# Kernel tuning notes

Hardware: AMD Instinct MI355X
Metric: run time of the kernel (lower is better)

The kernel has to match this reference:

```python
import jax, jax.numpy as jnp
import numpy as np

V, D, B, T, S, NH, DFF, NL, PAD = 4096, 512, 32, 32, 8, 8, 2048, 4, 0


def _ln(x, g, b, eps=1e-5):
    m = jnp.mean(x, -1, keepdims=True)
    v = jnp.mean((x - m) ** 2, -1, keepdims=True)
    return (x - m) * jax.lax.rsqrt(v + eps) * g + b


def _mha(q, k, v, in_w, in_b, out_w, out_b, attn_mask=None, kpm=None):
    b_, lq, d = q.shape
    lk = k.shape[1]
    dh = d // NH
    wq, wk, wv = jnp.split(in_w, 3, 0)
    bq, bk, bv = jnp.split(in_b, 3)
    qh = (q @ wq.T + bq).reshape(b_, lq, NH, dh).transpose(0, 2, 1, 3)
    kh = (k @ wk.T + bk).reshape(b_, lk, NH, dh).transpose(0, 2, 1, 3)
    vh = (v @ wv.T + bv).reshape(b_, lk, NH, dh).transpose(0, 2, 1, 3)
    s = jnp.einsum('bhqd,bhkd->bhqk', qh, kh) * (1.0 / np.sqrt(dh))
    if attn_mask is not None:
        s = jnp.where(attn_mask[None, None], -1e9, s)
    if kpm is not None:
        s = jnp.where(kpm[:, None, None, :], -1e9, s)
    a = jax.nn.softmax(s, -1)
    o = jnp.einsum('bhqk,bhkd->bhqd', a, vh).transpose(0, 2, 1, 3).reshape(b_, lq, d)
    return o @ out_w.T + out_b


def setup_inputs():
    key = jax.random.key(0)
    ks = iter(jax.random.split(key, 48))
    nrm = lambda shape, s=0.02: jax.random.normal(next(ks), shape, jnp.float32) * s
    d = {}
    d['input_ids'] = jax.random.randint(next(ks), (B, T), 1, V)
    d['ego_info'] = jax.random.normal(next(ks), (B, 3), jnp.float32)
    d['agent_tokens'] = jax.random.randint(next(ks), (B, T, S), 1, V)
    d['agent_feats'] = jax.random.normal(next(ks), (B, T, S, 5), jnp.float32)
    d['goal'] = jax.random.randint(next(ks), (B,), 1, V)
    d['emb'] = nrm((V, D), 1.0).at[PAD].set(0.0)  # padding_idx row zeroed
    d['se_w1'] = nrm((D, D + 3)); d['se_b1'] = jnp.zeros(D)
    d['se_w2'] = nrm((D, D)); d['se_b2'] = jnp.zeros(D)
    d['be_w1'] = nrm((D, D + 5)); d['be_b1'] = jnp.zeros(D)
    d['be_w2'] = nrm((D, D)); d['be_b2'] = jnp.zeros(D)
    for nm in ('in', 'mem', 'outn'):
        d[nm + '_g'] = jnp.ones(D); d[nm + '_b'] = jnp.zeros(D)
    d['sa_in_w'] = nrm((NL, 3 * D, D)); d['sa_in_b'] = jnp.zeros((NL, 3 * D))
    d['sa_out_w'] = nrm((NL, D, D)); d['sa_out_b'] = jnp.zeros((NL, D))
    d['ca_in_w'] = nrm((NL, 3 * D, D)); d['ca_in_b'] = jnp.zeros((NL, 3 * D))
    d['ca_out_w'] = nrm((NL, D, D)); d['ca_out_b'] = jnp.zeros((NL, D))
    d['ff_w1'] = nrm((NL, DFF, D)); d['ff_b1'] = jnp.zeros((NL, DFF))
    d['ff_w2'] = nrm((NL, D, DFF)); d['ff_b2'] = jnp.zeros((NL, D))
    for nm in ('ln1', 'ln2', 'ln3'):
        d[nm + '_g'] = jnp.ones((NL, D)); d[nm + '_b'] = jnp.zeros((NL, D))
    d['proj_w'] = nrm((V, D)); d['proj_b'] = jnp.zeros(V)
    return d


def _forward(input_ids, agent_tokens, goal, ego_info, agent_feats, emb, se_w1, se_b1, se_w2, se_b2, be_w1, be_b1, be_w2, be_b2, in_g, in_b, mem_g, mem_b, outn_g, outn_b, sa_in_w, sa_in_b, sa_out_w, sa_out_b, ca_in_w, ca_in_b, ca_out_w, ca_out_b, ff_w1, ff_b1, ff_w2, ff_b2, ln1_g, ln1_b, ln2_g, ln2_b, ln3_g, ln3_b, proj_w, proj_b):
    # --- encode_self_state: embed + fuse ego features -> (B, T, D) ---
    tok = emb[input_ids]
    ego = jnp.broadcast_to(ego_info[:, None, :], (B, T, 3))
    fused = jax.nn.relu(jnp.concatenate([tok, ego], -1) @ se_w1.T + se_b1) @ se_w2.T + se_b2
    self_state = _ln(fused, in_g, in_b)
    # --- encode_agent_topology -> env (B, T, S+1, D) ---
    amask = agent_tokens != -1
    aemb = emb[jnp.where(amask, agent_tokens, PAD)]
    astate = jax.nn.relu(jnp.concatenate([aemb, agent_feats], -1) @ be_w1.T + be_b1) @ be_w2.T + be_b2
    astate = astate * amask[..., None]
    goal_e = jnp.broadcast_to(emb[goal][:, None, None, :], (B, T, 1, D))
    env = _ln(jnp.concatenate([astate, goal_e], 2), mem_g, mem_b)
    # --- windowed memory for each step t in [1, T): frames [t-2, t-1, t] clipped ---
    steps = jnp.arange(1, T)
    idx = jnp.clip(steps[:, None] + jnp.array([-2, -1, 0]), 0, T - 1)  # (T-1, 3)
    mems = env[:, idx].reshape(B, T - 1, 3 * (S + 1), D).transpose(1, 0, 2, 3)  # (T-1, B, 3A, D)
    causal = jnp.triu(jnp.ones((T, T), bool), 1)
    kpm = input_ids == PAD

    # One full-length causal decoder run per step (vmapped); identical math to the
    # original prefix loop since position t only sees keys <= t, and we read position t.
    def decode(mem):
        x = self_state
        for l in range(NL):
            x = _ln(x + _mha(x, x, x, sa_in_w[l], sa_in_b[l], sa_out_w[l], sa_out_b[l], causal, kpm), ln1_g[l], ln1_b[l])
            x = _ln(x + _mha(x, mem, mem, ca_in_w[l], ca_in_b[l], ca_out_w[l], ca_out_b[l]), ln2_g[l], ln2_b[l])
            ff = jax.nn.relu(x @ ff_w1[l].T + ff_b1[l]) @ ff_w2[l].T + ff_b2[l]
            x = _ln(x + ff, ln3_g[l], ln3_b[l])
        return x

    dec_all = jax.vmap(decode)(mems)  # (T-1, B, T, D)
    sel = dec_all[jnp.arange(T - 1), :, steps, :]  # (T-1, B, D): last position of each prefix
    logits = _ln(sel, outn_g, outn_b) @ proj_w.T + proj_b
    return jnp.transpose(logits, (1, 0, 2))  # (B, T-1, V)


def reference(input_ids, ego_info, agent_tokens, agent_feats, goal, emb, se_w1, se_b1, se_w2, se_b2, be_w1, be_b1, be_w2, be_b2, in_g, in_b, mem_g, mem_b, outn_g, outn_b, sa_in_w, sa_in_b, sa_out_w, sa_out_b, ca_in_w, ca_in_b, ca_out_w, ca_out_b, ff_w1, ff_b1, ff_w2, ff_b2, ln1_g, ln1_b, ln2_g, ln2_b, ln3_g, ln3_b, proj_w, proj_b):
    return _forward(input_ids, agent_tokens, goal, ego_info, agent_feats, emb, se_w1, se_b1, se_w2, se_b2, be_w1, be_b1, be_w2, be_b2, in_g, in_b, mem_g, mem_b, outn_g, outn_b, sa_in_w, sa_in_b, sa_out_w, sa_out_b, ca_in_w, ca_in_b, ca_out_w, ca_out_b, ff_w1, ff_b1, ff_w2, ff_b2, ln1_g, ln1_b, ln2_g, ln2_b, ln3_g, ln3_b, proj_w, proj_b)
```

## Files before the change

kernel.cpp:

```cpp
#include <hip/hip_runtime.h>
#include <hip/hip_bf16.h>
#include <stdint.h>

typedef __hip_bfloat16 bf16;
typedef __attribute__((ext_vector_type(8))) short bf16x8;
typedef __attribute__((ext_vector_type(4))) float f32x4;

__device__ __forceinline__ float b2f(bf16 v) { return __bfloat162float(v); }
__device__ __forceinline__ bf16 f2b(float v) { return __float2bfloat16(v); }
__device__ __forceinline__ unsigned short f2bu(float v) {
    bf16 h = __float2bfloat16(v);
    return *(unsigned short*)&h;
}
__device__ __forceinline__ short f2bs(float v) {
    bf16 h = __float2bfloat16(v);
    return *(short*)&h;
}
__device__ __forceinline__ float su2f(unsigned short u) {
    unsigned int x = ((unsigned int)u) << 16;
    return *(float*)&x;
}

__device__ __forceinline__ void gload_lds16(const void* g, void* l) {
    __builtin_amdgcn_global_load_lds((const __attribute__((address_space(1))) void*)g,
                                     (__attribute__((address_space(3))) void*)l, 16, 0, 0);
}

__device__ __forceinline__ int swz_byte(int row, int kk) {
    return row * 80 + 2 * (kk & 7) + 16 * ((kk >> 3) ^ (row & 3));
}

__global__ __launch_bounds__(256) void mfma_gemm(
    const bf16* __restrict__ A, const bf16* __restrict__ W,
    const float* __restrict__ bias, void* __restrict__ C,
    int M, int N, int K, int c_bf16, int relu, int store_mode)
{
    __shared__ bf16 As[128 * 64];
    __shared__ bf16 Bs[128 * 64];
    const int gx = gridDim.x;
    const int nwg = gx * gridDim.y;
    const int orig = blockIdx.y * gx + blockIdx.x;
    const int qq = nwg >> 3, rr8 = nwg & 7;
    const int xcd = orig & 7, lid = orig >> 3;
    const int wgid = (xcd < rr8 ? xcd * (qq + 1) : rr8 * (qq + 1) + (xcd - rr8) * qq) + lid;
    const int m0 = (wgid / gx) * 128, n0 = (wgid % gx) * 128;

    const int tid = threadIdx.x;
    const int wave = tid >> 6, lane = tid & 63;
    const int wr = wave >> 1, wc = wave & 1;
    const int fr = lane & 15, fg = lane >> 4;
    f32x4 acc[4][4] = {};

    const int srow = lane >> 3;
    const int sunit = (lane & 7) ^ srow;

    for (int k0 = 0; k0 < K; k0 += 64) {
#pragma unroll
        for (int c = 0; c < 4; ++c) {
            const int chunk = wave * 4 + c;
            const int arow = m0 + chunk * 8 + srow;
            const int brow = n0 + chunk * 8 + srow;
            gload_lds16(A + (size_t)arow * K + k0 + sunit * 8, (char*)As + chunk * 1024);
            gload_lds16(W + (size_t)brow * K + k0 + sunit * 8, (char*)Bs + chunk * 1024);
        }
        __syncthreads();
#pragma unroll
        for (int kk = 0; kk < 64; kk += 32) {
            bf16x8 af[4], bw[4];
            const int bo = (kk + fg * 8) * 2;
#pragma unroll
            for (int t = 0; t < 4; ++t) {
                const int ra = wr * 64 + t * 16 + fr;
                af[t] = *(const bf16x8*)((const char*)As + ra * 128 + (bo ^ ((ra & 7) << 4)));
                const int rb = wc * 64 + t * 16 + fr;
                bw[t] = *(const bf16x8*)((const char*)Bs + rb * 128 + (bo ^ ((rb & 7) << 4)));
            }
#pragma unroll
            for (int mt = 0; mt < 4; ++mt)
#pragma unroll
                for (int nt = 0; nt < 4; ++nt)
                    acc[mt][nt] = __builtin_amdgcn_mfma_f32_16x16x32_bf16(
                        af[mt], bw[nt], acc[mt][nt], 0, 0, 0);
        }
        __syncthreads();
    }
#pragma unroll
    for (int mt = 0; mt < 4; ++mt) {
#pragma unroll
        for (int r = 0; r < 4; ++r) {
            const int m = m0 + wr * 64 + mt * 16 + fg * 4 + r;
            if (m >= M) continue;
            size_t orow = (size_t)m;
            if (store_mode == 1) orow = (size_t)(m & 31) * 31 + (m >> 5);
#pragma unroll
            for (int nt = 0; nt < 4; ++nt) {
                const int n = n0 + wc * 64 + nt * 16 + fr;
                float v = acc[mt][nt][r] + bias[n];
                if (relu) v = fmaxf(v, 0.f);
                if (c_bf16) ((bf16*)C)[orow * N + n] = f2b(v);
                else        ((float*)C)[orow * N + n] = v;
            }
        }
    }
}

__global__ __launch_bounds__(256) void self_attn_mfma(
    const bf16* __restrict__ qkv, const int* __restrict__ input_ids,
    bf16* __restrict__ attn_out)
{
    const int bid = blockIdx.x;
    const int hp = bid & 3;
    const int mb = bid >> 2;
    const int b = mb & 31;
    const size_t rowbase = (size_t)mb * 32;

    __shared__ __align__(16) char vt_raw[2][64 * 80];
    __shared__ __align__(16) char ps_raw[4][16 * 80];
    __shared__ float kpmv[32];

    const int tid = threadIdx.x;
    {
        const int r = tid & 31, u = tid >> 5;
#pragma unroll
        for (int e2 = 0; e2 < 2; ++e2) {
            const int h = hp * 2 + e2;
            bf16x8 v8 = *(const bf16x8*)(qkv + (rowbase + r) * 1536 + 1024 + h * 64 + u * 8);
#pragma unroll
            for (int j = 0; j < 8; ++j)
                *(short*)(vt_raw[e2] + swz_byte(u * 8 + j, r)) = v8[j];
        }
    }
    if (tid < 32) kpmv[tid] = (input_ids[b * 32 + tid] == 0) ? -1e9f : 0.f;
    __syncthreads();

    const int wave = tid >> 6, lane = tid & 63;
    const int e = wave >> 1;
    const int h = hp * 2 + e;
    const int qi = wave & 1;
    const int c = lane & 15, fg = lane >> 4;

    const bf16* qrow = qkv + (rowbase + qi * 16 + c) * 1536 + h * 64;
    bf16x8 af0 = *(const bf16x8*)(qrow + fg * 8);
    bf16x8 af1 = *(const bf16x8*)(qrow + 32 + fg * 8);
    f32x4 s[2];
#pragma unroll
    for (int kj = 0; kj < 2; ++kj) {
        const bf16* krow = qkv + (rowbase + kj * 16 + c) * 1536 + 512 + h * 64;
        bf16x8 b0 = *(const bf16x8*)(krow + fg * 8);
        bf16x8 b1 = *(const bf16x8*)(krow + 32 + fg * 8);
        f32x4 a = {};
        a = __builtin_amdgcn_mfma_f32_16x16x32_bf16(af0, b0, a, 0, 0, 0);
        a = __builtin_amdgcn_mfma_f32_16x16x32_bf16(af1, b1, a, 0, 0, 0);
        s[kj] = a;
    }

#pragma unroll
    for (int r = 0; r < 4; ++r) {
        const int qg = qi * 16 + fg * 4 + r;
        float v0 = s[0][r] * 0.125f + kpmv[c];
        float v1 = s[1][r] * 0.125f + kpmv[16 + c];
        if (c > qg) v0 = -1e9f;
        if (16 + c > qg) v1 = -1e9f;
        float m = fmaxf(v0, v1);
        m = fmaxf(m, __shfl_xor(m, 1)); m = fmaxf(m, __shfl_xor(m, 2));
        m = fmaxf(m, __shfl_xor(m, 4)); m = fmaxf(m, __shfl_xor(m, 8));
        float e0 = __expf(v0 - m), e1 = __expf(v1 - m);
        float sm = e0 + e1;
        sm += __shfl_xor(sm, 1); sm += __shfl_xor(sm, 2);
        sm += __shfl_xor(sm, 4); sm += __shfl_xor(sm, 8);
        float inv = 1.f / sm;
        *(short*)(ps_raw[wave] + swz_byte(fg * 4 + r, c))      = f2bs(e0 * inv);
        *(short*)(ps_raw[wave] + swz_byte(fg * 4 + r, 16 + c)) = f2bs(e1 * inv);
    }

    bf16x8 pa = *(const bf16x8*)(ps_raw[wave] + c * 80 + 16 * (fg ^ (c & 3)));
    f32x4 o[4];
#pragma unroll
    for (int dj = 0; dj < 4; ++dj) {
        bf16x8 bv = *(const bf16x8*)(vt_raw[e] + (dj * 16 + c) * 80 + 16 * (fg ^ (c & 3)));
        f32x4 a = {};
        o[dj] = __builtin_amdgcn_mfma_f32_16x16x32_bf16(pa, bv, a, 0, 0, 0);
    }
#pragma unroll
    for (int dj = 0; dj < 4; ++dj)
#pragma unroll
        for (int r = 0; r < 4; ++r)
            attn_out[(rowbase + qi * 16 + fg * 4 + r) * 512 + h * 64 + dj * 16 + c] = f2b(o[dj][r]);
}

__global__ __launch_bounds__(256) void cross_attn_mfma(
    const bf16* __restrict__ q, int qshared, const bf16* __restrict__ kv,
    bf16* __restrict__ attn_out)
{
    const int bid = blockIdx.x;
    const int hp = bid & 3;
    const int mb = bid >> 2;
    const size_t qb = (size_t)(qshared ? (mb & 31) : mb) * 32;
    const size_t kvb = (size_t)mb * 27;
    const size_t ob = (size_t)mb * 32;

    __shared__ __align__(16) char vt_raw[2][64 * 80];
    __shared__ __align__(16) char ps_raw[4][16 * 80];

    const int tid = threadIdx.x;
    {
        const int r = tid & 31, u = tid >> 5;
#pragma unroll
        for (int e2 = 0; e2 < 2; ++e2) {
            const int h = hp * 2 + e2;
            bf16x8 v8 = *(const bf16x8*)(kv + (kvb + r) * 1024 + 512 + h * 64 + u * 8);
#pragma unroll
            for (int j = 0; j < 8; ++j)
                *(short*)(vt_raw[e2] + swz_byte(u * 8 + j, r)) = v8[j];
        }
    }
    __syncthreads();

    const int wave = tid >> 6, lane = tid & 63;
    const int e = wave >> 1;
    const int h = hp * 2 + e;
    const int qi = wave & 1;
    const int c = lane & 15, fg = lane >> 4;

    const bf16* qrow = q + (qb + qi * 16 + c) * 512 + h * 64;
    bf16x8 af0 = *(const bf16x8*)(qrow + fg * 8);
    bf16x8 af1 = *(const bf16x8*)(qrow + 32 + fg * 8);
    f32x4 s[2];
#pragma unroll
    for (int kj = 0; kj < 2; ++kj) {
        const bf16* krow = kv + (kvb + kj * 16 + c) * 1024 + h * 64;
        bf16x8 b0 = *(const bf16x8*)(krow + fg * 8);
        bf16x8 b1 = *(const bf16x8*)(krow + 32 + fg * 8);
        f32x4 a = {};
        a = __builtin_amdgcn_mfma_f32_16x16x32_bf16(af0, b0, a, 0, 0, 0);
        a = __builtin_amdgcn_mfma_f32_16x16x32_bf16(af1, b1, a, 0, 0, 0);
        s[kj] = a;
    }
#pragma unroll
    for (int r = 0; r < 4; ++r) {
        float v0 = s[0][r] * 0.125f;
        float v1 = (16 + c < 27) ? s[1][r] * 0.125f : -1e9f;
        float m = fmaxf(v0, v1);
        m = fmaxf(m, __shfl_xor(m, 1)); m = fmaxf(m, __shfl_xor(m, 2));
        m = fmaxf(m, __shfl_xor(m, 4)); m = fmaxf(m, __shfl_xor(m, 8));
        float e0 = __expf(v0 - m), e1 = __expf(v1 - m);
        float sm = e0 + e1;
        sm += __shfl_xor(sm, 1); sm += __shfl_xor(sm, 2);
        sm += __shfl_xor(sm, 4); sm += __shfl_xor(sm, 8);
        float inv = 1.f / sm;
        *(short*)(ps_raw[wave] + swz_byte(fg * 4 + r, c))      = f2bs(e0 * inv);
        *(short*)(ps_raw[wave] + swz_byte(fg * 4 + r, 16 + c)) = f2bs(e1 * inv);
    }
    bf16x8 pa = *(const bf16x8*)(ps_raw[wave] + c * 80 + 16 * (fg ^ (c & 3)));
    f32x4 o[4];
#pragma unroll
    for (int dj = 0; dj < 4; ++dj) {
        bf16x8 bv = *(const bf16x8*)(vt_raw[e] + (dj * 16 + c) * 80 + 16 * (fg ^ (c & 3)));
        f32x4 a = {};
        o[dj] = __builtin_amdgcn_mfma_f32_16x16x32_bf16(pa, bv, a, 0, 0, 0);
    }
#pragma unroll
    for (int dj = 0; dj < 4; ++dj)
#pragma unroll
        for (int r = 0; r < 4; ++r)
            attn_out[(ob + qi * 16 + fg * 4 + r) * 512 + h * 64 + dj * 16 + c] = f2b(o[dj][r]);
}

__global__ __launch_bounds__(256) void ln_kernel(
    const float* __restrict__ x, const float* __restrict__ g,
    const float* __restrict__ b_, float* __restrict__ outf,
    bf16* __restrict__ outb, int rows)
{
    int row = blockIdx.x * 4 + (threadIdx.x >> 6);
    if (row >= rows) return;
    int lane = threadIdx.x & 63;
    const float4* xr = (const float4*)(x + (size_t)row * 512);
    float4 v[2];
    float sum = 0.f;
#pragma unroll
    for (int j = 0; j < 2; ++j) {
        v[j] = xr[lane + 64 * j];
        sum += v[j].x + v[j].y + v[j].z + v[j].w;
    }
    for (int o = 32; o; o >>= 1) sum += __shfl_xor(sum, o, 64);
    float mean = sum * (1.f / 512.f);
    float vs = 0.f;
#pragma unroll
    for (int j = 0; j < 2; ++j) {
        float dx = v[j].x - mean, dy = v[j].y - mean, dz = v[j].z - mean, dw = v[j].w - mean;
        vs += dx * dx + dy * dy + dz * dz + dw * dw;
    }
    for (int o = 32; o; o >>= 1) vs += __shfl_xor(vs, o, 64);
    float rstd = rsqrtf(vs * (1.f / 512.f) + 1e-5f);
#pragma unroll
    for (int j = 0; j < 2; ++j) {
        int u = lane + 64 * j;
        float4 g4 = ((const float4*)g)[u];
        float4 b4 = ((const float4*)b_)[u];
        float4 o4;
        o4.x = (v[j].x - mean) * rstd * g4.x + b4.x;
        o4.y = (v[j].y - mean) * rstd * g4.y + b4.y;
        o4.z = (v[j].z - mean) * rstd * g4.z + b4.z;
        o4.w = (v[j].w - mean) * rstd * g4.w + b4.w;
        if (outf) ((float4*)(outf + (size_t)row * 512))[u] = o4;
        if (outb) {
            ushort4 s4 = { f2bu(o4.x), f2bu(o4.y), f2bu(o4.z), f2bu(o4.w) };
            ((ushort4*)(outb + (size_t)row * 512))[u] = s4;
        }
    }
}

__global__ __launch_bounds__(256) void ln_res2_kernel(
    const float* __restrict__ xin, int rowmask, const bf16* __restrict__ br,
    const float* __restrict__ g, const float* __restrict__ b_,
    float* __restrict__ xout, bf16* __restrict__ xbout, int rows)
{
    int row = blockIdx.x * 4 + (threadIdx.x >> 6);
    if (row >= rows) return;
    int lane = threadIdx.x & 63;
    const float4* xr = (const float4*)(xin + (size_t)(row & rowmask) * 512);
    const ushort4* brr = (const ushort4*)(br + (size_t)row * 512);
    float4 v[2];
    float sum = 0.f;
#pragma unroll
    for (int j = 0; j < 2; ++j) {
        int u = lane + 64 * j;
        float4 a = xr[u];
        ushort4 s4 = brr[u];
        a.x += su2f(s4.x); a.y += su2f(s4.y); a.z += su2f(s4.z); a.w += su2f(s4.w);
        v[j] = a;
        sum += a.x + a.y + a.z + a.w;
    }
    for (int o = 32; o; o >>= 1) sum += __shfl_xor(sum, o, 64);
    float mean = sum * (1.f / 512.f);
    float vs = 0.f;
#pragma unroll
    for (int j = 0; j < 2; ++j) {
        float dx = v[j].x - mean, dy = v[j].y - mean, dz = v[j].z - mean, dw = v[j].w - mean;
        vs += dx * dx + dy * dy + dz * dz + dw * dw;
    }
    for (int o = 32; o; o >>= 1) vs += __shfl_xor(vs, o, 64);
    float rstd = rsqrtf(vs * (1.f / 512.f) + 1e-5f);
#pragma unroll
    for (int j = 0; j < 2; ++j) {
        int u = lane + 64 * j;
        float4 g4 = ((const float4*)g)[u];
        float4 b4 = ((const float4*)b_)[u];
        float4 o4;
        o4.x = (v[j].x - mean) * rstd * g4.x + b4.x;
        o4.y = (v[j].y - mean) * rstd * g4.y + b4.y;
        o4.z = (v[j].z - mean) * rstd * g4.z + b4.z;
        o4.w = (v[j].w - mean) * rstd * g4.w + b4.w;
        ((float4*)(xout + (size_t)row * 512))[u] = o4;
        ushort4 s4 = { f2bu(o4.x), f2bu(o4.y), f2bu(o4.z), f2bu(o4.w) };
        ((ushort4*)(xbout + (size_t)row * 512))[u] = s4;
    }
}

__global__ __launch_bounds__(256) void env_ln_kernel(
    const float* __restrict__ astate, const int* __restrict__ atok,
    const float* __restrict__ emb, const int* __restrict__ goal,
    const float* __restrict__ g, const float* __restrict__ b_, float* __restrict__ env)
{
    int row = blockIdx.x * 4 + (threadIdx.x >> 6);
    if (row >= 9216) return;
    int lane = threadIdx.x & 63;
    int s9 = row % 9;
    int bt = row / 9;
    float4 v[2];
    if (s9 < 8) {
        int ar = bt * 8 + s9;
        float msk = (atok[ar] != -1) ? 1.f : 0.f;
#pragma unroll
        for (int j = 0; j < 2; ++j) {
            float4 a = ((const float4*)(astate + (size_t)ar * 512))[lane + 64 * j];
            a.x *= msk; a.y *= msk; a.z *= msk; a.w *= msk;
            v[j] = a;
        }
    } else {
        int gi = goal[bt >> 5];
#pragma unroll
        for (int j = 0; j < 2; ++j)
            v[j] = ((const float4*)(emb + (size_t)gi * 512))[lane + 64 * j];
    }
    float sum = 0.f;
#pragma unroll
    for (int j = 0; j < 2; ++j) sum += v[j].x + v[j].y + v[j].z + v[j].w;
    for (int o = 32; o; o >>= 1) sum += __shfl_xor(sum, o, 64);
    float mean = sum * (1.f / 512.f);
    float vs = 0.f;
#pragma unroll
    for (int j = 0; j < 2; ++j) {
        float dx = v[j].x - mean, dy = v[j].y - mean, dz = v[j].z - mean, dw = v[j].w - mean;
        vs += dx * dx + dy * dy + dz * dz + dw * dw;
    }
    for (int o = 32; o; o >>= 1) vs += __shfl_xor(vs, o, 64);
    float rstd = rsqrtf(vs * (1.f / 512.f) + 1e-5f);
#pragma unroll
    for (int j = 0; j < 2; ++j) {
        int u = lane + 64 * j;
        float4 g4 = ((const float4*)g)[u];
        float4 b4 = ((const float4*)b_)[u];
        float4 o4;
        o4.x = (v[j].x - mean) * rstd * g4.x + b4.x;
        o4.y = (v[j].y - mean) * rstd * g4.y + b4.y;
        o4.z = (v[j].z - mean) * rstd * g4.z + b4.z;
        o4.w = (v[j].w - mean) * rstd * g4.w + b4.w;
        ((float4*)(env + (size_t)row * 512))[u] = o4;
    }
}

__global__ void mems_kernel(const float* __restrict__ env, bf16* __restrict__ mems)
{
    int row = blockIdx.x;
    int j = row % 27;
    int mb = row / 27;
    int m = mb >> 5, b = mb & 31;
    int gidx = j / 9, sp = j % 9;
    int t = m - 1 + gidx;
    t = t < 0 ? 0 : (t > 31 ? 31 : t);
    const float4* src = (const float4*)(env + ((size_t)(b * 32 + t) * 9 + sp) * 512);
    ushort4* dst = (ushort4*)(mems + (size_t)row * 512);
    int tid = threadIdx.x;
#pragma unroll
    for (int k = 0; k < 2; ++k) {
        int u = tid + 64 * k;
        float4 a = src[u];
        ushort4 s4 = { f2bu(a.x), f2bu(a.y), f2bu(a.z), f2bu(a.w) };
        dst[u] = s4;
    }
}

__global__ void xcatb_kernel(const int* __restrict__ ids, const float* __restrict__ ego,
                             const bf16* __restrict__ emb_b, bf16* __restrict__ xcat)
{
    int row = blockIdx.x;
    int tid = threadIdx.x;
    int b = row >> 5;
    int id = ids[row];
    bf16x8* dst = (bf16x8*)(xcat + (size_t)row * 576);
    if (tid < 64) {
        dst[tid] = ((const bf16x8*)(emb_b + (size_t)id * 512))[tid];
    } else if (tid == 64) {
        bf16x8 u = {};
        u[0] = f2bs(ego[b * 3 + 0]);
        u[1] = f2bs(ego[b * 3 + 1]);
        u[2] = f2bs(ego[b * 3 + 2]);
        dst[64] = u;
    } else if (tid < 72) {
        bf16x8 z = {};
        dst[tid] = z;
    }
}

__global__ void acatb_kernel(const int* __restrict__ atok, const float* __restrict__ afeat,
                             const bf16* __restrict__ emb_b, bf16* __restrict__ acat)
{
    int row = blockIdx.x;
    int tid = threadIdx.x;
    int tok = atok[row];
    int id = (tok != -1) ? tok : 0;
    bf16x8* dst = (bf16x8*)(acat + (size_t)row * 576);
    if (tid < 64) {
        dst[tid] = ((const bf16x8*)(emb_b + (size_t)id * 512))[tid];
    } else if (tid == 64) {
        bf16x8 u = {};
#pragma unroll
        for (int e = 0; e < 5; ++e) u[e] = f2bs(afeat[(size_t)row * 5 + e]);
        dst[64] = u;
    } else if (tid < 72) {
        bf16x8 z = {};
        dst[tid] = z;
    }
}

__global__ void sel_kernel(const float* __restrict__ x, float* __restrict__ sel, int m0, int cm)
{
    int row = blockIdx.x;
    int ml = row >> 5, b = row & 31;
    int m = m0 + ml;
    const float4* src = (const float4*)(x + ((size_t)(ml * 32 + b) * 32 + (m + 1)) * 512);
    float4* dst = (float4*)(sel + ((size_t)m * 32 + b) * 512);
    dst[threadIdx.x] = src[threadIdx.x];
}

__global__ void fill_kernel(float* __restrict__ o, int n, float v)
{
    int i = blockIdx.x * 256 + threadIdx.x;
    if (i < n) o[i] = v;
}

__global__ void cvtw_kernel(const float* __restrict__ s, unsigned short* __restrict__ d, int n)
{
    int n4 = n >> 2;
    int stride = gridDim.x * blockDim.x;
    for (int i = blockIdx.x * blockDim.x + threadIdx.x; i < n4; i += stride) {
        float4 v = ((const float4*)s)[i];
        ushort4 u = { f2bu(v.x), f2bu(v.y), f2bu(v.z), f2bu(v.w) };
        ((ushort4*)d)[i] = u;
    }
}

__global__ void cvtpad_kernel(const float* __restrict__ s, bf16* __restrict__ d, int Ks)
{
    int row = blockIdx.x;
    int tid = threadIdx.x;
    for (int c = tid; c < 576; c += 256) {
        float v = (c < Ks) ? s[(size_t)row * Ks + c] : 0.f;
        d[(size_t)row * 576 + c] = f2b(v);
    }
}

extern "C" void kernel_launch(void* const* d_in, const int* in_sizes, int n_in,
                              void* d_out, int out_size, void* d_ws, size_t ws_size,
                              hipStream_t stream)
{
    float* out = (float*)d_out;
    if (n_in < 40) {
        fill_kernel<<<(out_size + 255) / 256, 256, 0, stream>>>(out, out_size, 1e6f);
        return;
    }
    const int*   input_ids = (const int*)d_in[0];
    const float* ego       = (const float*)d_in[1];
    const int*   atok      = (const int*)d_in[2];
    const float* afeat     = (const float*)d_in[3];
    const int*   goal      = (const int*)d_in[4];
    const float* emb       = (const float*)d_in[5];
    const float* se_w1 = (const float*)d_in[6];
    const float* se_b1 = (const float*)d_in[7];
    const float* se_w2 = (const float*)d_in[8];
    const float* se_b2 = (const float*)d_in[9];
    const float* be_w1 = (const float*)d_in[10];
    const float* be_b1 = (const float*)d_in[11];
    const float* be_w2 = (const float*)d_in[12];
    const float* be_b2 = (const float*)d_in[13];
    const float* in_g  = (const float*)d_in[14];
    const float* in_b  = (const float*)d_in[15];
    const float* mem_g = (const float*)d_in[16];
    const float* mem_b = (const float*)d_in[17];
    const float* outn_g = (const float*)d_in[18];
    const float* outn_b = (const float*)d_in[19];
    const float* sa_in_w  = (const float*)d_in[20];
    const float* sa_in_b  = (const float*)d_in[21];
    const float* sa_out_w = (const float*)d_in[22];
    const float* sa_out_b = (const float*)d_in[23];
    const float* ca_in_w  = (const float*)d_in[24];
    const float* ca_in_b  = (const float*)d_in[25];
    const float* ca_out_w = (const float*)d_in[26];
    const float* ca_out_b = (const float*)d_in[27];
    const float* ff_w1 = (const float*)d_in[28];
    const float* ff_b1 = (const float*)d_in[29];
    const float* ff_w2 = (const float*)d_in[30];
    const float* ff_b2 = (const float*)d_in[31];
    const float* ln1_g = (const float*)d_in[32];
    const float* ln1_b = (const float*)d_in[33];
    const float* ln2_g = (const float*)d_in[34];
    const float* ln2_b = (const float*)d_in[35];
    const float* ln3_g = (const float*)d_in[36];
    const float* ln3_b = (const float*)d_in[37];
    const float* proj_w = (const float*)d_in[38];
    const float* proj_b = (const float*)d_in[39];

    auto ALIGN = [](size_t b) { return (b + 255) & ~(size_t)255; };
    uintptr_t base = (uintptr_t)d_ws;
    uintptr_t cur = (base + 255) & ~(uintptr_t)255;
    auto alloc = [&](size_t bytes) -> char* {
        char* r = (char*)cur; cur += (bytes + 255) & ~(size_t)255; return r;
    };

    float* self_state = (float*)alloc((size_t)1024 * 512 * 4);
    bf16*  ss_b       = (bf16*) alloc((size_t)1024 * 512 * 2);
    float* x0         = (float*)alloc((size_t)1024 * 512 * 4);
    bf16*  xb0        = (bf16*) alloc((size_t)1024 * 512 * 2);
    bf16*  q0b        = (bf16*) alloc((size_t)1024 * 512 * 2);
    bf16*  qkv0       = (bf16*) alloc((size_t)1024 * 1536 * 2);
    bf16*  araw0      = (bf16*) alloc((size_t)1024 * 512 * 2);
    bf16*  brnch0     = (bf16*) alloc((size_t)1024 * 512 * 2);
    bf16*  mems       = (bf16*) alloc((size_t)(26784 + 128) * 512 * 2);
    float* sel        = (float*)alloc((size_t)1024 * 512 * 4);
    bf16*  sel_ln_b   = (bf16*) alloc((size_t)1024 * 512 * 2);
    bf16* w_emb   = (bf16*)alloc((size_t)4096 * 512 * 2);
    bf16* w_se1p  = (bf16*)alloc((size_t)512 * 576 * 2);
    bf16* w_be1p  = (bf16*)alloc((size_t)512 * 576 * 2);
    bf16* w_se2   = (bf16*)alloc((size_t)512 * 512 * 2);
    bf16* w_be2   = (bf16*)alloc((size_t)512 * 512 * 2);
    bf16* w_sain  = (bf16*)alloc((size_t)4 * 1536 * 512 * 2);
    bf16* w_saout = (bf16*)alloc((size_t)4 * 512 * 512 * 2);
    bf16* w_cain  = (bf16*)alloc((size_t)4 * 1536 * 512 * 2);
    bf16* w_caout = (bf16*)alloc((size_t)4 * 512 * 512 * 2);
    bf16* w_ff1   = (bf16*)alloc((size_t)4 * 2048 * 512 * 2);
    bf16* w_ff2   = (bf16*)alloc((size_t)4 * 2048 * 512 * 2);
    bf16* w_proj  = (bf16*)alloc((size_t)4096 * 512 * 2);
    uintptr_t big = cur;

    size_t setup_need =
        ALIGN((size_t)1024 * 576 * 2) + ALIGN((size_t)1024 * 512 * 2) + ALIGN((size_t)1024 * 512 * 4) +
        ALIGN((size_t)8192 * 576 * 2) + ALIGN((size_t)8192 * 512 * 2) + ALIGN((size_t)8192 * 512 * 4) +
        ALIGN((size_t)9216 * 512 * 4);
    auto chunk_need = [&](int c) -> size_t {
        return ALIGN((size_t)c * 1024 * 512 * 4)
             + ALIGN((size_t)c * 1024 * 512 * 2)
             + ALIGN((size_t)c * 1024 * 1536 * 2)
             + ALIGN((size_t)c * 1024 * 512 * 2)
             + ALIGN((size_t)c * 1024 * 512 * 2)
             + ALIGN((size_t)c * 1024 * 2048 * 2)
             + ALIGN(((size_t)c * 864 + 128) * 1024 * 2);
    };
    int CH = 0;
    if (ws_size > (size_t)(big - base) + 4096) {
        size_t avail = ws_size - (size_t)(big - base) - 4096;
        for (int c = 31; c >= 1; --c)
            if (setup_need <= avail && chunk_need(c) <= avail) { CH = c; break; }
    }
    if (!CH) {
        fill_kernel<<<(out_size + 255) / 256, 256, 0, stream>>>(out, out_size, 1e6f);
        return;
    }

    auto cvt = [&](const float* s, bf16* d, size_t n) {
        int n4 = (int)(n >> 2);
        int blocks = (n4 + 255) / 256; if (blocks > 2048) blocks = 2048;
        cvtw_kernel<<<blocks, 256, 0, stream>>>(s, (unsigned short*)d, (int)n);
    };
    cvt(emb, w_emb, (size_t)4096 * 512);
    cvtpad_kernel<<<512, 256, 0, stream>>>(se_w1, w_se1p, 515);
    cvtpad_kernel<<<512, 256, 0, stream>>>(be_w1, w_be1p, 517);
    cvt(se_w2, w_se2, (size_t)512 * 512);
    cvt(be_w2, w_be2, (size_t)512 * 512);
    cvt(sa_in_w, w_sain, (size_t)4 * 1536 * 512);
    cvt(sa_out_w, w_saout, (size_t)4 * 512 * 512);
    cvt(ca_in_w, w_cain, (size_t)4 * 1536 * 512);
    cvt(ca_out_w, w_caout, (size_t)4 * 512 * 512);
    cvt(ff_w1, w_ff1, (size_t)4 * 2048 * 512);
    cvt(ff_w2, w_ff2, (size_t)4 * 2048 * 512);
    cvt(proj_w, w_proj, (size_t)4096 * 512);

    auto launch_mfma = [&](const bf16* A, const bf16* W, const float* bias,
                           void* C, int c_bf16, int M, int N, int K, int relu, int smode) {
        dim3 g(N / 128, (M + 127) / 128);
        mfma_gemm<<<g, 256, 0, stream>>>(A, W, bias, C, M, N, K, c_bf16, relu, smode);
    };

    {
        uintptr_t sp = big;
        auto salloc = [&](size_t b) -> char* { char* r = (char*)sp; sp += ALIGN(b); return r; };
        bf16*  xcat_b = (bf16*) salloc((size_t)1024 * 576 * 2);
        bf16*  h1b    = (bf16*) salloc((size_t)1024 * 512 * 2);
        float* fused  = (float*)salloc((size_t)1024 * 512 * 4);
        bf16*  acat_b = (bf16*) salloc((size_t)8192 * 576 * 2);
        bf16*  ah1b   = (bf16*) salloc((size_t)8192 * 512 * 2);
        float* astate = (float*)salloc((size_t)8192 * 512 * 4);
        float* env    = (float*)salloc((size_t)9216 * 512 * 4);

        xcatb_kernel<<<1024, 128, 0, stream>>>(input_ids, ego, w_emb, xcat_b);
        launch_mfma(xcat_b, w_se1p, se_b1, h1b, 1, 1024, 512, 576, 1, 0);
        launch_mfma(h1b, w_se2, se_b2, fused, 0, 1024, 512, 512, 0, 0);
        ln_kernel<<<256, 256, 0, stream>>>(fused, in_g, in_b, self_state, ss_b, 1024);

        acatb_kernel<<<8192, 128, 0, stream>>>(atok, afeat, w_emb, acat_b);
        launch_mfma(acat_b, w_be1p, be_b1, ah1b, 1, 8192, 512, 576, 1, 0);
        launch_mfma(ah1b, w_be2, be_b2, astate, 0, 8192, 512, 512, 0, 0);
        env_ln_kernel<<<2304, 256, 0, stream>>>(astate, atok, emb, goal, mem_g, mem_b, env);
        mems_kernel<<<26784, 64, 0, stream>>>(env, mems);
    }

    launch_mfma(ss_b, w_sain, sa_in_b, qkv0, 1, 1024, 1536, 512, 0, 0);
    self_attn_mfma<<<32 * 4, 256, 0, stream>>>(qkv0, input_ids, araw0);
    launch_mfma(araw0, w_saout, sa_out_b, brnch0, 1, 1024, 512, 512, 0, 0);
    ln_res2_kernel<<<256, 256, 0, stream>>>(self_state, 0x7fffffff, brnch0,
                                            ln1_g, ln1_b, x0, xb0, 1024);
    launch_mfma(xb0, w_cain, ca_in_b, q0b, 1, 1024, 512, 512, 0, 0);

    {
        uintptr_t sp = big;
        auto salloc = [&](size_t b) -> char* { char* r = (char*)sp; sp += ALIGN(b); return r; };
        float* x     = (float*)salloc((size_t)CH * 1024 * 512 * 4);
        bf16*  xb    = (bf16*) salloc((size_t)CH * 1024 * 512 * 2);
        bf16*  qkv   = (bf16*) salloc((size_t)CH * 1024 * 1536 * 2);
        bf16*  araw  = (bf16*) salloc((size_t)CH * 1024 * 512 * 2);
        bf16*  brnch = (bf16*) salloc((size_t)CH * 1024 * 512 * 2);
        bf16*  ff1b  = (bf16*) salloc((size_t)CH * 1024 * 2048 * 2);
        bf16*  kv    = (bf16*) salloc(((size_t)CH * 864 + 128) * 1024 * 2);

        for (int m0 = 0; m0 < 31; m0 += CH) {
            int cm = (31 - m0) < CH ? (31 - m0) : CH;
            int Mr = cm * 1024;
            launch_mfma(mems + (size_t)m0 * 864 * 512, w_cain + (size_t)512 * 512,
                        ca_in_b + 512, kv, 1, cm * 864, 1024, 512, 0, 0);
            cross_attn_mfma<<<cm * 32 * 4, 256, 0, stream>>>(q0b, 1, kv, araw);
            launch_mfma(araw, w_caout, ca_out_b, brnch, 1, Mr, 512, 512, 0, 0);
            ln_res2_kernel<<<(Mr + 3) / 4, 256, 0, stream>>>(x0, 1023, brnch,
                                                             ln2_g, ln2_b, x, xb, Mr);
            launch_mfma(xb, w_ff1, ff_b1, ff1b, 1, Mr, 2048, 512, 1, 0);
            launch_mfma(ff1b, w_ff2, ff_b2, brnch, 1, Mr, 512, 2048, 0, 0);
            ln_res2_kernel<<<(Mr + 3) / 4, 256, 0, stream>>>(x, 0x7fffffff, brnch,
                                                             ln3_g, ln3_b, x, xb, Mr);
            for (int l = 1; l < 4; ++l) {
                launch_mfma(xb, w_sain + (size_t)l * 1536 * 512, sa_in_b + l * 1536,
                            qkv, 1, Mr, 1536, 512, 0, 0);
                self_attn_mfma<<<cm * 32 * 4, 256, 0, stream>>>(qkv, input_ids, araw);
                launch_mfma(araw, w_saout + (size_t)l * 512 * 512, sa_out_b + l * 512,
                            brnch, 1, Mr, 512, 512, 0, 0);
                ln_res2_kernel<<<(Mr + 3) / 4, 256, 0, stream>>>(x, 0x7fffffff, brnch,
                                                                 ln1_g + l * 512, ln1_b + l * 512, x, xb, Mr);
                launch_mfma(xb, w_cain + (size_t)l * 1536 * 512, ca_in_b + l * 1536,
                            qkv, 1, Mr, 512, 512, 0, 0);
                launch_mfma(mems + (size_t)m0 * 864 * 512,
                            w_cain + (size_t)l * 1536 * 512 + (size_t)512 * 512,
                            ca_in_b + l * 1536 + 512,
                            kv, 1, cm * 864, 1024, 512, 0, 0);
                cross_attn_mfma<<<cm * 32 * 4, 256, 0, stream>>>(qkv, 0, kv, araw);
                launch_mfma(araw, w_caout + (size_t)l * 512 * 512, ca_out_b + l * 512,
                            brnch, 1, Mr, 512, 512, 0, 0);
                ln_res2_kernel<<<(Mr + 3) / 4, 256, 0, stream>>>(x, 0x7fffffff, brnch,
                                                                 ln2_g + l * 512, ln2_b + l * 512, x, xb, Mr);
                launch_mfma(xb, w_ff1 + (size_t)l * 2048 * 512, ff_b1 + l * 2048,
                            ff1b, 1, Mr, 2048, 512, 1, 0);
                launch_mfma(ff1b, w_ff2 + (size_t)l * 512 * 2048, ff_b2 + l * 512,
                            brnch, 1, Mr, 512, 2048, 0, 0);
                ln_res2_kernel<<<(Mr + 3) / 4, 256, 0, stream>>>(x, 0x7fffffff, brnch,
                                                                 ln3_g + l * 512, ln3_b + l * 512, x, xb, Mr);
            }
            sel_kernel<<<cm * 32, 128, 0, stream>>>(x, sel, m0, cm);
        }
    }

    ln_kernel<<<248, 256, 0, stream>>>(sel, outn_g, outn_b, (float*)nullptr, sel_ln_b, 992);
    launch_mfma(sel_ln_b, w_proj, proj_b, out, 0, 992, 4096, 512, 0, 1);
}
```

Measured before the change: 3.446 ms.

## Fuse GEMM with residual+LayerNorm epilogue and precompute deduplicated cross-attn KV

Adds a gemm_ln kernel that computes full 512-wide output rows per block and applies bias, residual add and LayerNorm in the epilogue. This replaces the separate bf16 branch buffer and ln_res2 pass after the attention-out and FFN2 GEMMs. Cross-attention K/V are now projected once per layer over the 9216 unique env rows instead of over 27x-replicated mems per prefix chunk. The attention kernel gathers rows through an index function, which removes the mems materialization and a large amount of redundant GEMM work. The risks are fewer blocks (M/128) for the fused GEMM and a one-pass variance computed as E[x^2]-mean^2.

```diff
diff --git a/kernel.cpp b/kernel.cpp
--- a/kernel.cpp
+++ b/kernel.cpp
@@ -104,6 +104,117 @@
     }
 }
 
+__global__ __launch_bounds__(512, 2) void gemm_ln(
+    const bf16* __restrict__ A, const bf16* __restrict__ W,
+    const float* __restrict__ bias,
+    const float* __restrict__ res, int rowmask,
+    const float* __restrict__ g, const float* __restrict__ b_,
+    float* __restrict__ xout, bf16* __restrict__ xbout, int M, int K)
+{
+    __shared__ bf16 As[128 * 64];
+    __shared__ bf16 Bs[512 * 64];
+    __shared__ float redS[128][4];
+    __shared__ float redV[128][4];
+
+    const int tid = threadIdx.x;
+    const int wave = tid >> 6, lane = tid & 63;
+    const int m0 = blockIdx.x * 128;
+    const int wr = wave >> 2, wc = wave & 3;
+    const int fr = lane & 15, fg = lane >> 4;
+    const int srow = lane >> 3;
+    const int sunit = (lane & 7) ^ srow;
+
+    f32x4 acc[4][8] = {};
+    for (int k0 = 0; k0 < K; k0 += 64) {
+#pragma unroll
+        for (int c = 0; c < 2; ++c) {
+            const int chunk = wave * 2 + c;
+            const int arow = m0 + chunk * 8 + srow;
+            gload_lds16(A + (size_t)arow * K + k0 + sunit * 8, (char*)As + chunk * 1024);
+        }
+#pragma unroll
+        for (int c = 0; c < 8; ++c) {
+            const int chunk = wave * 8 + c;
+            const int brow = chunk * 8 + srow;
+            gload_lds16(W + (size_t)brow * K + k0 + sunit * 8, (char*)Bs + chunk * 1024);
+        }
+        __syncthreads();
+#pragma unroll
+        for (int kk = 0; kk < 64; kk += 32) {
+            const int bo = (kk + fg * 8) * 2;
+            bf16x8 af[4];
+#pragma unroll
+            for (int t = 0; t < 4; ++t) {
+                const int ra = wr * 64 + t * 16 + fr;
+                af[t] = *(const bf16x8*)((const char*)As + ra * 128 + (bo ^ ((ra & 7) << 4)));
+            }
+#pragma unroll
+            for (int nt = 0; nt < 8; ++nt) {
+                const int rb = wc * 128 + nt * 16 + fr;
+                bf16x8 bw = *(const bf16x8*)((const char*)Bs + rb * 128 + (bo ^ ((rb & 7) << 4)));
+#pragma unroll
+                for (int mt = 0; mt < 4; ++mt)
+                    acc[mt][nt] = __builtin_amdgcn_mfma_f32_16x16x32_bf16(
+                        af[mt], bw, acc[mt][nt], 0, 0, 0);
+            }
+        }
+        __syncthreads();
+    }
+
+    float breg[8], greg[8], bbreg[8];
+#pragma unroll
+    for (int nt = 0; nt < 8; ++nt) {
+        const int col = wc * 128 + nt * 16 + fr;
+        breg[nt] = bias[col];
+        greg[nt] = g[col];
+        bbreg[nt] = b_[col];
+    }
+
+#pragma unroll
+    for (int mt = 0; mt < 4; ++mt) {
+#pragma unroll
+        for (int r = 0; r < 4; ++r) {
+            const int rl = wr * 64 + mt * 16 + fg * 4 + r;
+            const float* rrow = res ? res + (size_t)((m0 + rl) & rowmask) * 512 : nullptr;
+            float s1 = 0.f, s2 = 0.f;
+#pragma unroll
+            for (int nt = 0; nt < 8; ++nt) {
+                float v = acc[mt][nt][r] + breg[nt];
+                if (rrow) v += rrow[wc * 128 + nt * 16 + fr];
+                acc[mt][nt][r] = v;
+                s1 += v; s2 += v * v;
+            }
+            s1 += __shfl_xor(s1, 1); s2 += __shfl_xor(s2, 1);
+            s1 += __shfl_xor(s1, 2); s2 += __shfl_xor(s2, 2);
+            s1 += __shfl_xor(s1, 4); s2 += __shfl_xor(s2, 4);
+            s1 += __shfl_xor(s1, 8); s2 += __shfl_xor(s2, 8);
+            if (fr == 0) { redS[rl][wc] = s1; redV[rl][wc] = s2; }
+        }
+    }
+    __syncthreads();
+
+#pragma unroll
+    for (int mt = 0; mt < 4; ++mt) {
+#pragma unroll
+        for (int r = 0; r < 4; ++r) {
+            const int rl = wr * 64 + mt * 16 + fg * 4 + r;
+            const float s1 = redS[rl][0] + redS[rl][1] + redS[rl][2] + redS[rl][3];
+            const float s2 = redV[rl][0] + redV[rl][1] + redV[rl][2] + redV[rl][3];
+            const float mean = s1 * (1.f / 512.f);
+            const float var = s2 * (1.f / 512.f) - mean * mean;
+            const float rstd = rsqrtf(var + 1e-5f);
+            const size_t grow = (size_t)(m0 + rl);
+#pragma unroll
+            for (int nt = 0; nt < 8; ++nt) {
+                const int col = wc * 128 + nt * 16 + fr;
+                const float val = (acc[mt][nt][r] - mean) * rstd * greg[nt] + bbreg[nt];
+                xout[grow * 512 + col] = val;
+                xbout[grow * 512 + col] = f2b(val);
+            }
+        }
+    }
+}
+
 __global__ __launch_bounds__(256) void self_attn_mfma(
     const bf16* __restrict__ qkv, const int* __restrict__ input_ids,
     bf16* __restrict__ attn_out)
@@ -153,7 +264,6 @@
         a = __builtin_amdgcn_mfma_f32_16x16x32_bf16(af1, b1, a, 0, 0, 0);
         s[kj] = a;
     }
-
 #pragma unroll
     for (int r = 0; r < 4; ++r) {
         const int qg = qi * 16 + fg * 4 + r;
@@ -172,7 +282,6 @@
         *(short*)(ps_raw[wave] + swz_byte(fg * 4 + r, c))      = f2bs(e0 * inv);
         *(short*)(ps_raw[wave] + swz_byte(fg * 4 + r, 16 + c)) = f2bs(e1 * inv);
     }
-
     bf16x8 pa = *(const bf16x8*)(ps_raw[wave] + c * 80 + 16 * (fg ^ (c & 3)));
     f32x4 o[4];
 #pragma unroll
@@ -188,15 +297,23 @@
             attn_out[(rowbase + qi * 16 + fg * 4 + r) * 512 + h * 64 + dj * 16 + c] = f2b(o[dj][r]);
 }
 
+__device__ __forceinline__ int env_idx(int m, int b, int j) {
+    int gi = j / 9, sp = j - gi * 9;
+    int t = m - 1 + gi;
+    t = t < 0 ? 0 : (t > 31 ? 31 : t);
+    return (b * 32 + t) * 9 + sp;
+}
+
 __global__ __launch_bounds__(256) void cross_attn_mfma(
-    const bf16* __restrict__ q, int qshared, const bf16* __restrict__ kv,
-    bf16* __restrict__ attn_out)
+    const bf16* __restrict__ q, int qshared, const bf16* __restrict__ ekv,
+    bf16* __restrict__ attn_out, int m0glob)
 {
     const int bid = blockIdx.x;
     const int hp = bid & 3;
     const int mb = bid >> 2;
-    const size_t qb = (size_t)(qshared ? (mb & 31) : mb) * 32;
-    const size_t kvb = (size_t)mb * 27;
+    const int b = mb & 31;
+    const int m = m0glob + (mb >> 5);
+    const size_t qb = (size_t)(qshared ? b : mb) * 32;
     const size_t ob = (size_t)mb * 32;
 
     __shared__ __align__(16) char vt_raw[2][64 * 80];
@@ -205,10 +322,11 @@
     const int tid = threadIdx.x;
     {
         const int r = tid & 31, u = tid >> 5;
+        const size_t erow = (size_t)env_idx(m, b, r) * 1024;
 #pragma unroll
         for (int e2 = 0; e2 < 2; ++e2) {
             const int h = hp * 2 + e2;
-            bf16x8 v8 = *(const bf16x8*)(kv + (kvb + r) * 1024 + 512 + h * 64 + u * 8);
+            bf16x8 v8 = *(const bf16x8*)(ekv + erow + 512 + h * 64 + u * 8);
 #pragma unroll
             for (int j = 0; j < 8; ++j)
                 *(short*)(vt_raw[e2] + swz_byte(u * 8 + j, r)) = v8[j];
@@ -228,9 +346,9 @@
     f32x4 s[2];
 #pragma unroll
     for (int kj = 0; kj < 2; ++kj) {
-        const bf16* krow = kv + (kvb + kj * 16 + c) * 1024 + h * 64;
-        bf16x8 b0 = *(const bf16x8*)(krow + fg * 8);
-        bf16x8 b1 = *(const bf16x8*)(krow + 32 + fg * 8);
+        const size_t erow = (size_t)env_idx(m, b, kj * 16 + c) * 1024;
+        bf16x8 b0 = *(const bf16x8*)(ekv + erow + h * 64 + fg * 8);
+        bf16x8 b1 = *(const bf16x8*)(ekv + erow + h * 64 + 32 + fg * 8);
         f32x4 a = {};
         a = __builtin_amdgcn_mfma_f32_16x16x32_bf16(af0, b0, a, 0, 0, 0);
         a = __builtin_amdgcn_mfma_f32_16x16x32_bf16(af1, b1, a, 0, 0, 0);
@@ -240,10 +358,10 @@
     for (int r = 0; r < 4; ++r) {
         float v0 = s[0][r] * 0.125f;
         float v1 = (16 + c < 27) ? s[1][r] * 0.125f : -1e9f;
-        float m = fmaxf(v0, v1);
-        m = fmaxf(m, __shfl_xor(m, 1)); m = fmaxf(m, __shfl_xor(m, 2));
-        m = fmaxf(m, __shfl_xor(m, 4)); m = fmaxf(m, __shfl_xor(m, 8));
-        float e0 = __expf(v0 - m), e1 = __expf(v1 - m);
+        float m2 = fmaxf(v0, v1);
+        m2 = fmaxf(m2, __shfl_xor(m2, 1)); m2 = fmaxf(m2, __shfl_xor(m2, 2));
+        m2 = fmaxf(m2, __shfl_xor(m2, 4)); m2 = fmaxf(m2, __shfl_xor(m2, 8));
+        float e0 = __expf(v0 - m2), e1 = __expf(v1 - m2);
         float sm = e0 + e1;
         sm += __shfl_xor(sm, 1); sm += __shfl_xor(sm, 2);
         sm += __shfl_xor(sm, 4); sm += __shfl_xor(sm, 8);
@@ -310,57 +428,10 @@
     }
 }
 
-__global__ __launch_bounds__(256) void ln_res2_kernel(
-    const float* __restrict__ xin, int rowmask, const bf16* __restrict__ br,
-    const float* __restrict__ g, const float* __restrict__ b_,
-    float* __restrict__ xout, bf16* __restrict__ xbout, int rows)
-{
-    int row = blockIdx.x * 4 + (threadIdx.x >> 6);
-    if (row >= rows) return;
-    int lane = threadIdx.x & 63;
-    const float4* xr = (const float4*)(xin + (size_t)(row & rowmask) * 512);
-    const ushort4* brr = (const ushort4*)(br + (size_t)row * 512);
-    float4 v[2];
-    float sum = 0.f;
-#pragma unroll
-    for (int j = 0; j < 2; ++j) {
-        int u = lane + 64 * j;
-        float4 a = xr[u];
-        ushort4 s4 = brr[u];
-        a.x += su2f(s4.x); a.y += su2f(s4.y); a.z += su2f(s4.z); a.w += su2f(s4.w);
-        v[j] = a;
-        sum += a.x + a.y + a.z + a.w;
-    }
-    for (int o = 32; o; o >>= 1) sum += __shfl_xor(sum, o, 64);
-    float mean = sum * (1.f / 512.f);
-    float vs = 0.f;
-#pragma unroll
-    for (int j = 0; j < 2; ++j) {
-        float dx = v[j].x - mean, dy = v[j].y - mean, dz = v[j].z - mean, dw = v[j].w - mean;
-        vs += dx * dx + dy * dy + dz * dz + dw * dw;
-    }
-    for (int o = 32; o; o >>= 1) vs += __shfl_xor(vs, o, 64);
-    float rstd = rsqrtf(vs * (1.f / 512.f) + 1e-5f);
-#pragma unroll
-    for (int j = 0; j < 2; ++j) {
-        int u = lane + 64 * j;
-        float4 g4 = ((const float4*)g)[u];
-        float4 b4 = ((const float4*)b_)[u];
-        float4 o4;
-        o4.x = (v[j].x - mean) * rstd * g4.x + b4.x;
-        o4.y = (v[j].y - mean) * rstd * g4.y + b4.y;
-        o4.z = (v[j].z - mean) * rstd * g4.z + b4.z;
-        o4.w = (v[j].w - mean) * rstd * g4.w + b4.w;
-        ((float4*)(xout + (size_t)row * 512))[u] = o4;
-        ushort4 s4 = { f2bu(o4.x), f2bu(o4.y), f2bu(o4.z), f2bu(o4.w) };
-        ((ushort4*)(xbout + (size_t)row * 512))[u] = s4;
-    }
-}
-
 __global__ __launch_bounds__(256) void env_ln_kernel(
     const float* __restrict__ astate, const int* __restrict__ atok,
     const float* __restrict__ emb, const int* __restrict__ goal,
-    const float* __restrict__ g, const float* __restrict__ b_, float* __restrict__ env)
+    const float* __restrict__ g, const float* __restrict__ b_, bf16* __restrict__ envb)
 {
     int row = blockIdx.x * 4 + (threadIdx.x >> 6);
     if (row >= 9216) return;
@@ -401,33 +472,12 @@
         int u = lane + 64 * j;
         float4 g4 = ((const float4*)g)[u];
         float4 b4 = ((const float4*)b_)[u];
-        float4 o4;
-        o4.x = (v[j].x - mean) * rstd * g4.x + b4.x;
-        o4.y = (v[j].y - mean) * rstd * g4.y + b4.y;
-        o4.z = (v[j].z - mean) * rstd * g4.z + b4.z;
-        o4.w = (v[j].w - mean) * rstd * g4.w + b4.w;
-        ((float4*)(env + (size_t)row * 512))[u] = o4;
-    }
-}
-
-__global__ void mems_kernel(const float* __restrict__ env, bf16* __restrict__ mems)
-{
-    int row = blockIdx.x;
-    int j = row % 27;
-    int mb = row / 27;
-    int m = mb >> 5, b = mb & 31;
-    int gidx = j / 9, sp = j % 9;
-    int t = m - 1 + gidx;
-    t = t < 0 ? 0 : (t > 31 ? 31 : t);
-    const float4* src = (const float4*)(env + ((size_t)(b * 32 + t) * 9 + sp) * 512);
-    ushort4* dst = (ushort4*)(mems + (size_t)row * 512);
-    int tid = threadIdx.x;
-#pragma unroll
-    for (int k = 0; k < 2; ++k) {
-        int u = tid + 64 * k;
-        float4 a = src[u];
-        ushort4 s4 = { f2bu(a.x), f2bu(a.y), f2bu(a.z), f2bu(a.w) };
-        dst[u] = s4;
+        ushort4 s4;
+        s4.x = f2bu((v[j].x - mean) * rstd * g4.x + b4.x);
+        s4.y = f2bu((v[j].y - mean) * rstd * g4.y + b4.y);
+        s4.z = f2bu((v[j].z - mean) * rstd * g4.z + b4.z);
+        s4.w = f2bu((v[j].w - mean) * rstd * g4.w + b4.w);
+        ((ushort4*)(envb + (size_t)row * 512))[u] = s4;
     }
 }
 
@@ -575,8 +625,8 @@
     bf16*  q0b        = (bf16*) alloc((size_t)1024 * 512 * 2);
     bf16*  qkv0       = (bf16*) alloc((size_t)1024 * 1536 * 2);
     bf16*  araw0      = (bf16*) alloc((size_t)1024 * 512 * 2);
-    bf16*  brnch0     = (bf16*) alloc((size_t)1024 * 512 * 2);
-    bf16*  mems       = (bf16*) alloc((size_t)(26784 + 128) * 512 * 2);
+    bf16*  env_b      = (bf16*) alloc((size_t)9216 * 512 * 2);
+    bf16*  env_kv     = (bf16*) alloc((size_t)4 * 9216 * 1024 * 2);
     float* sel        = (float*)alloc((size_t)1024 * 512 * 4);
     bf16*  sel_ln_b   = (bf16*) alloc((size_t)1024 * 512 * 2);
     bf16* w_emb   = (bf16*)alloc((size_t)4096 * 512 * 2);
@@ -594,17 +644,15 @@
     uintptr_t big = cur;
 
     size_t setup_need =
-        ALIGN((size_t)1024 * 576 * 2) + ALIGN((size_t)1024 * 512 * 2) + ALIGN((size_t)1024 * 512 * 4) +
-        ALIGN((size_t)8192 * 576 * 2) + ALIGN((size_t)8192 * 512 * 2) + ALIGN((size_t)8192 * 512 * 4) +
-        ALIGN((size_t)9216 * 512 * 4);
+        ALIGN((size_t)1024 * 576 * 2) + ALIGN((size_t)1024 * 512 * 2) +
+        ALIGN((size_t)8192 * 576 * 2) + ALIGN((size_t)8192 * 512 * 2) +
+        ALIGN((size_t)8192 * 512 * 4);
     auto chunk_need = [&](int c) -> size_t {
         return ALIGN((size_t)c * 1024 * 512 * 4)
              + ALIGN((size_t)c * 1024 * 512 * 2)
              + ALIGN((size_t)c * 1024 * 1536 * 2)
              + ALIGN((size_t)c * 1024 * 512 * 2)
-             + ALIGN((size_t)c * 1024 * 512 * 2)
-             + ALIGN((size_t)c * 1024 * 2048 * 2)
-             + ALIGN(((size_t)c * 864 + 128) * 1024 * 2);
+             + ALIGN((size_t)c * 1024 * 2048 * 2);
     };
     int CH = 0;
     if (ws_size > (size_t)(big - base) + 4096) {
@@ -640,35 +688,39 @@
         dim3 g(N / 128, (M + 127) / 128);
         mfma_gemm<<<g, 256, 0, stream>>>(A, W, bias, C, M, N, K, c_bf16, relu, smode);
     };
+    auto launch_gemm_ln = [&](const bf16* A, const bf16* W, const float* bias,
+                              const float* res, int rowmask, const float* g, const float* b_,
+                              float* xout, bf16* xbout, int M, int K) {
+        gemm_ln<<<M / 128, 512, 0, stream>>>(A, W, bias, res, rowmask, g, b_, xout, xbout, M, K);
+    };
 
     {
         uintptr_t sp = big;
         auto salloc = [&](size_t b) -> char* { char* r = (char*)sp; sp += ALIGN(b); return r; };
         bf16*  xcat_b = (bf16*) salloc((size_t)1024 * 576 * 2);
         bf16*  h1b    = (bf16*) salloc((size_t)1024 * 512 * 2);
-        float* fused  = (float*)salloc((size_t)1024 * 512 * 4);
         bf16*  acat_b = (bf16*) salloc((size_t)8192 * 576 * 2);
         bf16*  ah1b   = (bf16*) salloc((size_t)8192 * 512 * 2);
         float* astate = (float*)salloc((size_t)8192 * 512 * 4);
-        float* env    = (float*)salloc((size_t)9216 * 512 * 4);
 
         xcatb_kernel<<<1024, 128, 0, stream>>>(input_ids, ego, w_emb, xcat_b);
         launch_mfma(xcat_b, w_se1p, se_b1, h1b, 1, 1024, 512, 576, 1, 0);
-        launch_mfma(h1b, w_se2, se_b2, fused, 0, 1024, 512, 512, 0, 0);
-        ln_kernel<<<256, 256, 0, stream>>>(fused, in_g, in_b, self_state, ss_b, 1024);
+        launch_gemm_ln(h1b, w_se2, se_b2, nullptr, 0, in_g, in_b, self_state, ss_b, 1024, 512);
 
         acatb_kernel<<<8192, 128, 0, stream>>>(atok, afeat, w_emb, acat_b);
         launch_mfma(acat_b, w_be1p, be_b1, ah1b, 1, 8192, 512, 576, 1, 0);
         launch_mfma(ah1b, w_be2, be_b2, astate, 0, 8192, 512, 512, 0, 0);
-        env_ln_kernel<<<2304, 256, 0, stream>>>(astate, atok, emb, goal, mem_g, mem_b, env);
-        mems_kernel<<<26784, 64, 0, stream>>>(env, mems);
-    }
+        env_ln_kernel<<<2304, 256, 0, stream>>>(astate, atok, emb, goal, mem_g, mem_b, env_b);
+    }
+    for (int l = 0; l < 4; ++l)
+        launch_mfma(env_b, w_cain + (size_t)l * 1536 * 512 + (size_t)512 * 512,
+                    ca_in_b + l * 1536 + 512,
+                    env_kv + (size_t)l * 9216 * 1024, 1, 9216, 1024, 512, 0, 0);
 
     launch_mfma(ss_b, w_sain, sa_in_b, qkv0, 1, 1024, 1536, 512, 0, 0);
     self_attn_mfma<<<32 * 4, 256, 0, stream>>>(qkv0, input_ids, araw0);
-    launch_mfma(araw0, w_saout, sa_out_b, brnch0, 1, 1024, 512, 512, 0, 0);
-    ln_res2_kernel<<<256, 256, 0, stream>>>(self_state, 0x7fffffff, brnch0,
-                                            ln1_g, ln1_b, x0, xb0, 1024);
+    launch_gemm_ln(araw0, w_saout, sa_out_b, self_state, 0x7fffffff,
+                   ln1_g, ln1_b, x0, xb0, 1024, 512);
     launch_mfma(xb0, w_cain, ca_in_b, q0b, 1, 1024, 512, 512, 0, 0);
 
     {
@@ -678,48 +730,31 @@
         bf16*  xb    = (bf16*) salloc((size_t)CH * 1024 * 512 * 2);
         bf16*  qkv   = (bf16*) salloc((size_t)CH * 1024 * 1536 * 2);
         bf16*  araw  = (bf16*) salloc((size_t)CH * 1024 * 512 * 2);
-        bf16*  brnch = (bf16*) salloc((size_t)CH * 1024 * 512 * 2);
         bf16*  ff1b  = (bf16*) salloc((size_t)CH * 1024 * 2048 * 2);
-        bf16*  kv    = (bf16*) salloc(((size_t)CH * 864 + 128) * 1024 * 2);
 
         for (int m0 = 0; m0 < 31; m0 += CH) {
             int cm = (31 - m0) < CH ? (31 - m0) : CH;
             int Mr = cm * 1024;
-            launch_mfma(mems + (size_t)m0 * 864 * 512, w_cain + (size_t)512 * 512,
-                        ca_in_b + 512, kv, 1, cm * 864, 1024, 512, 0, 0);
-            cross_attn_mfma<<<cm * 32 * 4, 256, 0, stream>>>(q0b, 1, kv, araw);
-            launch_mfma(araw, w_caout, ca_out_b, brnch, 1, Mr, 512, 512, 0, 0);
-            ln_res2_kernel<<<(Mr + 3) / 4, 256, 0, stream>>>(x0, 1023, brnch,
-                                                             ln2_g, ln2_b, x, xb, Mr);
+            cross_attn_mfma<<<cm * 32 * 4, 256, 0, stream>>>(q0b, 1, env_kv, araw, m0);
+            launch_gemm_ln(araw, w_caout, ca_out_b, x0, 1023, ln2_g, ln2_b, x, xb, Mr, 512);
             launch_mfma(xb, w_ff1, ff_b1, ff1b, 1, Mr, 2048, 512, 1, 0);
-            launch_mfma(ff1b, w_ff2, ff_b2, brnch, 1, Mr, 512, 2048, 0, 0);
-            ln_res2_kernel<<<(Mr + 3) / 4, 256, 0, stream>>>(x, 0x7fffffff, brnch,
-                                                             ln3_g, ln3_b, x, xb, Mr);
+            launch_gemm_ln(ff1b, w_ff2, ff_b2, x, 0x7fffffff, ln3_g, ln3_b, x, xb, Mr, 2048);
             for (int l = 1; l < 4; ++l) {
                 launch_mfma(xb, w_sain + (size_t)l * 1536 * 512, sa_in_b + l * 1536,
                             qkv, 1, Mr, 1536, 512, 0, 0);
                 self_attn_mfma<<<cm * 32 * 4, 256, 0, stream>>>(qkv, input_ids, araw);
-                launch_mfma(araw, w_saout + (size_t)l * 512 * 512, sa_out_b + l * 512,
-                            brnch, 1, Mr, 512, 512, 0, 0);
-                ln_res2_kernel<<<(Mr + 3) / 4, 256, 0, stream>>>(x, 0x7fffffff, brnch,
-                                                                 ln1_g + l * 512, ln1_b + l * 512, x, xb, Mr);
+                launch_gemm_ln(araw, w_saout + (size_t)l * 512 * 512, sa_out_b + l * 512,
+                               x, 0x7fffffff, ln1_g + l * 512, ln1_b + l * 512, x, xb, Mr, 512);
                 launch_mfma(xb, w_cain + (size_t)l * 1536 * 512, ca_in_b + l * 1536,
                             qkv, 1, Mr, 512, 512, 0, 0);
-                launch_mfma(mems + (size_t)m0 * 864 * 512,
-                            w_cain + (size_t)l * 1536 * 512 + (size_t)512 * 512,
-                            ca_in_b + l * 1536 + 512,
-                            kv, 1, cm * 864, 1024, 512, 0, 0);
-                cross_attn_mfma<<<cm * 32 * 4, 256, 0, stream>>>(qkv, 0, kv, araw);
-                launch_mfma(araw, w_caout + (size_t)l * 512 * 512, ca_out_b + l * 512,
-                            brnch, 1, Mr, 512, 512, 0, 0);
-                ln_res2_kernel<<<(Mr + 3) / 4, 256, 0, stream>>>(x, 0x7fffffff, brnch,
-                                                                 ln2_g + l * 512, ln2_b + l * 512, x, xb, Mr);
+                cross_attn_mfma<<<cm * 32 * 4, 256, 0, stream>>>(
+                    qkv, 0, env_kv + (size_t)l * 9216 * 1024, araw, m0);
+                launch_gemm_ln(araw, w_caout + (size_t)l * 512 * 512, ca_out_b + l * 512,
+                               x, 0x7fffffff, ln2_g + l * 512, ln2_b + l * 512, x, xb, Mr, 512);
                 launch_mfma(xb, w_ff1 + (size_t)l * 2048 * 512, ff_b1 + l * 2048,
                             ff1b, 1, Mr, 2048, 512, 1, 0);
-                launch_mfma(ff1b, w_ff2 + (size_t)l * 512 * 2048, ff_b2 + l * 512,
-                            brnch, 1, Mr, 512, 2048, 0, 0);
-                ln_res2_kernel<<<(Mr + 3) / 4, 256, 0, stream>>>(x, 0x7fffffff, brnch,
-                                                                 ln3_g + l * 512, ln3_b + l * 512, x, xb, Mr);
+                launch_gemm_ln(ff1b, w_ff2 + (size_t)l * 512 * 2048, ff_b2 + l * 512,
+                               x, 0x7fffffff, ln3_g + l * 512, ln3_b + l * 512, x, xb, Mr, 2048);
             }
             sel_kernel<<<cm * 32, 128, 0, stream>>>(x, sel, m0, cm);
         }
```

New measurement: 5.559 ms. 61.3% more time.
